# Kernel optimization log

Measured on AMD Instinct MI355X. Metric: run time of the kernel, lower is better.

The kernel has to match this reference:

```python
import jax, jax.numpy as jnp
import numpy as np

H, W = 1024, 2048
PS, ST = 16, 8          # patch_size, stride (init kwargs)
MARGIN = 1e-4           # margin from nerfstudio depth_ranking_loss
NH = (H - PS) // ST + 1  # 127
NW = (W - PS) // ST + 1  # 255
P = NH * NW             # 32385 patches
N = PS * PS             # 256 pixels per patch


def setup_inputs() -> dict:
    key = jax.random.key(0)
    k1, k2, k3, k4 = jax.random.split(key, 4)
    pred = jax.random.normal(k1, (1, 1, H, W), dtype=jnp.float32)
    target = jax.random.normal(k2, (1, 1, H, W), dtype=jnp.float32)
    mask = jax.random.bernoulli(k3, 0.5, (1, 1, H, W))
    # per-patch randomness standing in for torch.randperm: argsort of this
    # noise restricted to valid pixels is a uniform random permutation of
    # the masked (valid) pixel list.
    perm_noise = jax.random.uniform(k4, (P, N), dtype=jnp.float32)
    return {"pred": pred, "target": target, "mask": mask, "perm_noise": perm_noise}


def _extract_patches(x):
    # x: [H, W] -> [P, N] overlapping PSxPS patches with stride ST (scan order)
    i0 = jnp.arange(0, H - PS + 1, ST)           # [NH]
    j0 = jnp.arange(0, W - PS + 1, ST)           # [NW]
    ii = i0[:, None] + jnp.arange(PS)[None, :]   # [NH, PS]
    jj = j0[:, None] + jnp.arange(PS)[None, :]   # [NW, PS]
    g = x[ii[:, None, :, None], jj[None, :, None, :]]  # [NH, NW, PS, PS]
    return g.reshape(P, N)


def reference(pred, target, mask, perm_noise):
    pp = _extract_patches(pred[0, 0])            # [P, N]
    tp = _extract_patches(target[0, 0])          # [P, N]
    mp = _extract_patches(mask[0, 0])            # [P, N] bool

    # rank of each valid pixel in scan order (torch: pred_patch[mask] ordering)
    rank = jnp.cumsum(mp.astype(jnp.int32), axis=1) - 1        # [P, N]
    # random permutation of valid pixels: valid pixels sorted by noise come first
    noise = jnp.where(mp, perm_noise, jnp.inf)
    order = jnp.argsort(noise, axis=1)                          # [P, N]
    # valid pixel with scan-rank r pairs with order[r] (a random valid pixel)
    partner = jnp.take_along_axis(order, jnp.clip(rank, 0, N - 1), axis=1)

    dt = tp - jnp.take_along_axis(tp, partner, axis=1)
    dp = pp - jnp.take_along_axis(pp, partner, axis=1) + MARGIN

    # depth_ranking_loss: penalize pairs whose signs disagree, loss = mean |dp|
    sel = mp & (jnp.sign(dt) != jnp.sign(dp))
    cnt = jnp.sum(sel, axis=1).astype(pp.dtype)                 # [P]
    patch_loss = jnp.sum(jnp.where(sel, jnp.abs(dp), 0.0), axis=1) / cnt

    has_valid = jnp.any(mp, axis=1)                             # skip empty-mask patches
    n_used = jnp.sum(has_valid).astype(pp.dtype)
    return jnp.sum(jnp.where(has_valid, patch_loss, 0.0)) / n_used
```

## Files before the change

### kernel.cpp

```cpp
#include <hip/hip_runtime.h>
#include <cstdint>

#define H 1024
#define W 2048
#define PS 16
#define ST 8
#define NHH ((H - PS) / ST + 1)
#define NWW ((W - PS) / ST + 1)
#define NPATCH (NHH * NWW)
#define NN 256
#define MARGIN 1e-4f
#define RED_BLOCKS 128
#define WPB 4

#define WS_LOSS_OFF   0
#define WS_VALID_OFF  131072
#define WS_ACC_OFF    262144

__global__ void detect_init_kernel(const unsigned int* __restrict__ mw,
                                   unsigned int* __restrict__ wsacc) {
    if (threadIdx.x < 4) wsacc[threadIdx.x] = 0u;
    __syncthreads();
    unsigned int w = mw[threadIdx.x];
    if (w > 1u) atomicOr((int*)(wsacc + 3), 1);
}

__device__ __forceinline__ int resolve_rank(const unsigned* __restrict__ slot,
                                            const unsigned* __restrict__ baseA,
                                            const unsigned* __restrict__ endA,
                                            unsigned key) {
    const unsigned hi = key >> 23;
    const unsigned b  = baseA[hi];
    const unsigned e  = endA[hi];
    int rk = (int)b;
    for (unsigned j = b; j < e; ++j) rk += (int)(slot[j] < key);
    return rk;
}

__global__ __launch_bounds__(256) void patch_loss_kernel(
    const float* __restrict__ pred, const float* __restrict__ target,
    const void* __restrict__ mask, const float* __restrict__ noise,
    const int* __restrict__ byteflag,
    float* __restrict__ out_loss, float* __restrict__ out_valid)
{
    __shared__ float sP[WPB][NN];
    __shared__ float sT[WPB][NN];
    __shared__ unsigned sHist[WPB][NN];
    __shared__ unsigned sBase[WPB][NN];
    __shared__ unsigned sSlot[WPB][NN];
    __shared__ unsigned short sOrder[WPB][NN];

    const int tid  = threadIdx.x;
    const int lane = tid & 63;
    const int wid  = tid >> 6;
    const int p = blockIdx.x * WPB + wid;
    if (p >= NPATCH) return;

    const int ih = p / NWW;
    const int iw = p - ih * NWW;
    const int e0  = lane << 2;
    const int row = e0 >> 4;
    const int col = e0 & 15;
    const int pix = (ih * ST + row) * W + iw * ST + col;

    const float4 pv = *(const float4*)(pred + pix);
    const float4 tv = *(const float4*)(target + pix);
    const float4 nz = *(const float4*)(noise + p * NN + e0);

    int m0, m1, m2, m3;
    if (*byteflag) {
        const unsigned mw_ = *(const unsigned*)((const unsigned char*)mask + pix);
        m0 = (mw_ & 0x000000FFu) != 0; m1 = (mw_ & 0x0000FF00u) != 0;
        m2 = (mw_ & 0x00FF0000u) != 0; m3 = (mw_ & 0xFF000000u) != 0;
    } else {
        const int4 mv = *(const int4*)((const int*)mask + pix);
        m0 = mv.x != 0; m1 = mv.y != 0; m2 = mv.z != 0; m3 = mv.w != 0;
    }
    const int localcnt = m0 + m1 + m2 + m3;

    int incl = localcnt;
#pragma unroll
    for (int d = 1; d < 64; d <<= 1) {
        const int t = __shfl_up(incl, d);
        if (lane >= d) incl += t;
    }
    const int cnt = __shfl(incl, 63);
    const int r0 = incl - localcnt;
    const int r1 = r0 + m0;
    const int r2 = r1 + m1;
    const int r3 = r2 + m2;

    *(float4*)&sP[wid][e0] = pv;
    *(float4*)&sT[wid][e0] = tv;

    const unsigned k0 = ((__float_as_uint(nz.x + 1.0f) - 0x3F800000u) << 8) | (unsigned)(e0 + 0);
    const unsigned k1 = ((__float_as_uint(nz.y + 1.0f) - 0x3F800000u) << 8) | (unsigned)(e0 + 1);
    const unsigned k2 = ((__float_as_uint(nz.z + 1.0f) - 0x3F800000u) << 8) | (unsigned)(e0 + 2);
    const unsigned k3 = ((__float_as_uint(nz.w + 1.0f) - 0x3F800000u) << 8) | (unsigned)(e0 + 3);

    *(uint4*)&sHist[wid][e0] = make_uint4(0u, 0u, 0u, 0u);
    __builtin_amdgcn_wave_barrier();
    if (m0) atomicAdd(&sHist[wid][k0 >> 23], 1u);
    if (m1) atomicAdd(&sHist[wid][k1 >> 23], 1u);
    if (m2) atomicAdd(&sHist[wid][k2 >> 23], 1u);
    if (m3) atomicAdd(&sHist[wid][k3 >> 23], 1u);
    __builtin_amdgcn_wave_barrier();

    const uint4 hq = *(uint4*)&sHist[wid][e0];
    const unsigned lsum = hq.x + hq.y + hq.z + hq.w;
    int hincl = (int)lsum;
#pragma unroll
    for (int d = 1; d < 64; d <<= 1) {
        const int t = __shfl_up(hincl, d);
        if (lane >= d) hincl += t;
    }
    const unsigned b0 = (unsigned)hincl - lsum;
    const unsigned b1 = b0 + hq.x;
    const unsigned b2 = b1 + hq.y;
    const unsigned b3 = b2 + hq.z;
    const uint4 bq = make_uint4(b0, b1, b2, b3);
    *(uint4*)&sHist[wid][e0] = bq;
    *(uint4*)&sBase[wid][e0] = bq;
    __builtin_amdgcn_wave_barrier();

    if (m0) { const unsigned s = atomicAdd(&sHist[wid][k0 >> 23], 1u); sSlot[wid][s] = k0; }
    if (m1) { const unsigned s = atomicAdd(&sHist[wid][k1 >> 23], 1u); sSlot[wid][s] = k1; }
    if (m2) { const unsigned s = atomicAdd(&sHist[wid][k2 >> 23], 1u); sSlot[wid][s] = k2; }
    if (m3) { const unsigned s = atomicAdd(&sHist[wid][k3 >> 23], 1u); sSlot[wid][s] = k3; }
    __builtin_amdgcn_wave_barrier();

    if (m0) sOrder[wid][resolve_rank(sSlot[wid], sBase[wid], sHist[wid], k0)] = (unsigned short)(k0 & 0xFFu);
    if (m1) sOrder[wid][resolve_rank(sSlot[wid], sBase[wid], sHist[wid], k1)] = (unsigned short)(k1 & 0xFFu);
    if (m2) sOrder[wid][resolve_rank(sSlot[wid], sBase[wid], sHist[wid], k2)] = (unsigned short)(k2 & 0xFFu);
    if (m3) sOrder[wid][resolve_rank(sSlot[wid], sBase[wid], sHist[wid], k3)] = (unsigned short)(k3 & 0xFFu);
    __builtin_amdgcn_wave_barrier();

    float la = 0.0f;
    int   lc = 0;
    if (m0) {
        const int pa = sOrder[wid][r0];
        const float dt = tv.x - sT[wid][pa];
        const float dp = pv.x - sP[wid][pa] + MARGIN;
        if (((dt > 0.0f) - (dt < 0.0f)) != ((dp > 0.0f) - (dp < 0.0f))) { la += fabsf(dp); ++lc; }
    }
    if (m1) {
        const int pa = sOrder[wid][r1];
        const float dt = tv.y - sT[wid][pa];
        const float dp = pv.y - sP[wid][pa] + MARGIN;
        if (((dt > 0.0f) - (dt < 0.0f)) != ((dp > 0.0f) - (dp < 0.0f))) { la += fabsf(dp); ++lc; }
    }
    if (m2) {
        const int pa = sOrder[wid][r2];
        const float dt = tv.z - sT[wid][pa];
        const float dp = pv.z - sP[wid][pa] + MARGIN;
        if (((dt > 0.0f) - (dt < 0.0f)) != ((dp > 0.0f) - (dp < 0.0f))) { la += fabsf(dp); ++lc; }
    }
    if (m3) {
        const int pa = sOrder[wid][r3];
        const float dt = tv.w - sT[wid][pa];
        const float dp = pv.w - sP[wid][pa] + MARGIN;
        if (((dt > 0.0f) - (dt < 0.0f)) != ((dp > 0.0f) - (dp < 0.0f))) { la += fabsf(dp); ++lc; }
    }

    float lcf = (float)lc;
#pragma unroll
    for (int off = 32; off > 0; off >>= 1) {
        la  += __shfl_down(la, off);
        lcf += __shfl_down(lcf, off);
    }
    if (lane == 0) {
        float pl = 0.0f, hv = 0.0f;
        if (cnt > 0) { pl = la / lcf; hv = 1.0f; }
        out_loss[p]  = pl;
        out_valid[p] = hv;
    }
}

__global__ __launch_bounds__(256) void reduce_finalize_kernel(
    const float* __restrict__ loss, const float* __restrict__ valid,
    float* __restrict__ acc, unsigned int* __restrict__ ticket,
    float* __restrict__ out)
{
    __shared__ float sa[4], sb[4];
    float a = 0.0f, b = 0.0f;
    for (int i = blockIdx.x * blockDim.x + threadIdx.x; i < NPATCH;
         i += gridDim.x * blockDim.x) {
        a += loss[i];
        b += valid[i];
    }
    for (int off = 32; off > 0; off >>= 1) {
        a += __shfl_down(a, off);
        b += __shfl_down(b, off);
    }
    const int lane = threadIdx.x & 63, wid = threadIdx.x >> 6;
    if (lane == 0) { sa[wid] = a; sb[wid] = b; }
    __syncthreads();
    if (threadIdx.x == 0) {
        atomicAdd(&acc[0], sa[0] + sa[1] + sa[2] + sa[3]);
        atomicAdd(&acc[1], sb[0] + sb[1] + sb[2] + sb[3]);
        __threadfence();
        const unsigned int old = atomicAdd(ticket, 1u);
        if (old == (unsigned int)(gridDim.x - 1)) {
            const float s = atomicAdd(&acc[0], 0.0f);
            const float c = atomicAdd(&acc[1], 0.0f);
            out[0] = s / c;
        }
    }
}

extern "C" void kernel_launch(void* const* d_in, const int* in_sizes, int n_in,
                              void* d_out, int out_size, void* d_ws, size_t ws_size,
                              hipStream_t stream) {
    const float* pred   = (const float*)d_in[0];
    const float* target = (const float*)d_in[1];
    const void*  mask   = d_in[2];
    const float* noise  = (const float*)d_in[3];

    char* ws = (char*)d_ws;
    float*        ws_loss  = (float*)(ws + WS_LOSS_OFF);
    float*        ws_valid = (float*)(ws + WS_VALID_OFF);
    float*        acc      = (float*)(ws + WS_ACC_OFF);
    unsigned int* ticket   = (unsigned int*)(ws + WS_ACC_OFF + 8);
    int*          flag     = (int*)(ws + WS_ACC_OFF + 12);

    const int nblocks = (NPATCH + WPB - 1) / WPB;
    detect_init_kernel<<<1, 1024, 0, stream>>>((const unsigned int*)mask,
                                               (unsigned int*)acc);
    patch_loss_kernel<<<nblocks, 256, 0, stream>>>(pred, target, mask, noise,
                                                   flag, ws_loss, ws_valid);
    reduce_finalize_kernel<<<RED_BLOCKS, 256, 0, stream>>>(ws_loss, ws_valid,
                                                           acc, ticket,
                                                           (float*)d_out);
}
```

Baseline: 118.6 us.

## Fuse per-patch reduction via slotted atomics and pack histogram base/end in shared

```diff
diff --git a/kernel.cpp b/kernel.cpp
--- a/kernel.cpp
+++ b/kernel.cpp
@@ -10,28 +10,28 @@
 #define NPATCH (NHH * NWW)
 #define NN 256
 #define MARGIN 1e-4f
-#define RED_BLOCKS 128
 #define WPB 4
-
-#define WS_LOSS_OFF   0
-#define WS_VALID_OFF  131072
-#define WS_ACC_OFF    262144
+#define NSLOT 128
+#define SLOT_STRIDE 8
+
+#define WS_VALID_F 1024
+#define WS_FLAG_F  2048
 
 __global__ void detect_init_kernel(const unsigned int* __restrict__ mw,
-                                   unsigned int* __restrict__ wsacc) {
-    if (threadIdx.x < 4) wsacc[threadIdx.x] = 0u;
+                                   float* __restrict__ wsf) {
+    ((float2*)wsf)[threadIdx.x] = make_float2(0.0f, 0.0f);
+    if (threadIdx.x == 0) ((int*)wsf)[WS_FLAG_F] = 0;
     __syncthreads();
-    unsigned int w = mw[threadIdx.x];
-    if (w > 1u) atomicOr((int*)(wsacc + 3), 1);
+    const unsigned int w = mw[threadIdx.x];
+    if (w > 1u) atomicOr((int*)wsf + WS_FLAG_F, 1);
 }
 
 __device__ __forceinline__ int resolve_rank(const unsigned* __restrict__ slot,
-                                            const unsigned* __restrict__ baseA,
-                                            const unsigned* __restrict__ endA,
+                                            const unsigned* __restrict__ histp,
                                             unsigned key) {
-    const unsigned hi = key >> 23;
-    const unsigned b  = baseA[hi];
-    const unsigned e  = endA[hi];
+    const unsigned w = histp[key >> 23];
+    const unsigned b = w >> 16;
+    const unsigned e = w & 0xFFFFu;
     int rk = (int)b;
     for (unsigned j = b; j < e; ++j) rk += (int)(slot[j] < key);
     return rk;
@@ -41,12 +41,11 @@
     const float* __restrict__ pred, const float* __restrict__ target,
     const void* __restrict__ mask, const float* __restrict__ noise,
     const int* __restrict__ byteflag,
-    float* __restrict__ out_loss, float* __restrict__ out_valid)
+    float* __restrict__ lossAcc, float* __restrict__ validAcc)
 {
     __shared__ float sP[WPB][NN];
     __shared__ float sT[WPB][NN];
     __shared__ unsigned sHist[WPB][NN];
-    __shared__ unsigned sBase[WPB][NN];
     __shared__ unsigned sSlot[WPB][NN];
     __shared__ unsigned short sOrder[WPB][NN];
 
@@ -118,21 +117,20 @@
     const unsigned b1 = b0 + hq.x;
     const unsigned b2 = b1 + hq.y;
     const unsigned b3 = b2 + hq.z;
-    const uint4 bq = make_uint4(b0, b1, b2, b3);
-    *(uint4*)&sHist[wid][e0] = bq;
-    *(uint4*)&sBase[wid][e0] = bq;
-    __builtin_amdgcn_wave_barrier();
-
-    if (m0) { const unsigned s = atomicAdd(&sHist[wid][k0 >> 23], 1u); sSlot[wid][s] = k0; }
-    if (m1) { const unsigned s = atomicAdd(&sHist[wid][k1 >> 23], 1u); sSlot[wid][s] = k1; }
-    if (m2) { const unsigned s = atomicAdd(&sHist[wid][k2 >> 23], 1u); sSlot[wid][s] = k2; }
-    if (m3) { const unsigned s = atomicAdd(&sHist[wid][k3 >> 23], 1u); sSlot[wid][s] = k3; }
-    __builtin_amdgcn_wave_barrier();
-
-    if (m0) sOrder[wid][resolve_rank(sSlot[wid], sBase[wid], sHist[wid], k0)] = (unsigned short)(k0 & 0xFFu);
-    if (m1) sOrder[wid][resolve_rank(sSlot[wid], sBase[wid], sHist[wid], k1)] = (unsigned short)(k1 & 0xFFu);
-    if (m2) sOrder[wid][resolve_rank(sSlot[wid], sBase[wid], sHist[wid], k2)] = (unsigned short)(k2 & 0xFFu);
-    if (m3) sOrder[wid][resolve_rank(sSlot[wid], sBase[wid], sHist[wid], k3)] = (unsigned short)(k3 & 0xFFu);
+    *(uint4*)&sHist[wid][e0] = make_uint4((b0 << 16) | b0, (b1 << 16) | b1,
+                                          (b2 << 16) | b2, (b3 << 16) | b3);
+    __builtin_amdgcn_wave_barrier();
+
+    if (m0) { const unsigned s = atomicAdd(&sHist[wid][k0 >> 23], 1u) & 0xFFFFu; sSlot[wid][s] = k0; }
+    if (m1) { const unsigned s = atomicAdd(&sHist[wid][k1 >> 23], 1u) & 0xFFFFu; sSlot[wid][s] = k1; }
+    if (m2) { const unsigned s = atomicAdd(&sHist[wid][k2 >> 23], 1u) & 0xFFFFu; sSlot[wid][s] = k2; }
+    if (m3) { const unsigned s = atomicAdd(&sHist[wid][k3 >> 23], 1u) & 0xFFFFu; sSlot[wid][s] = k3; }
+    __builtin_amdgcn_wave_barrier();
+
+    if (m0) sOrder[wid][resolve_rank(sSlot[wid], sHist[wid], k0)] = (unsigned short)(k0 & 0xFFu);
+    if (m1) sOrder[wid][resolve_rank(sSlot[wid], sHist[wid], k1)] = (unsigned short)(k1 & 0xFFu);
+    if (m2) sOrder[wid][resolve_rank(sSlot[wid], sHist[wid], k2)] = (unsigned short)(k2 & 0xFFu);
+    if (m3) sOrder[wid][resolve_rank(sSlot[wid], sHist[wid], k3)] = (unsigned short)(k3 & 0xFFu);
     __builtin_amdgcn_wave_barrier();
 
     float la = 0.0f;
@@ -168,44 +166,25 @@
         la  += __shfl_down(la, off);
         lcf += __shfl_down(lcf, off);
     }
-    if (lane == 0) {
-        float pl = 0.0f, hv = 0.0f;
-        if (cnt > 0) { pl = la / lcf; hv = 1.0f; }
-        out_loss[p]  = pl;
-        out_valid[p] = hv;
-    }
-}
-
-__global__ __launch_bounds__(256) void reduce_finalize_kernel(
-    const float* __restrict__ loss, const float* __restrict__ valid,
-    float* __restrict__ acc, unsigned int* __restrict__ ticket,
-    float* __restrict__ out)
-{
-    __shared__ float sa[4], sb[4];
-    float a = 0.0f, b = 0.0f;
-    for (int i = blockIdx.x * blockDim.x + threadIdx.x; i < NPATCH;
-         i += gridDim.x * blockDim.x) {
-        a += loss[i];
-        b += valid[i];
-    }
+    if (lane == 0 && cnt > 0) {
+        const int slot = (p & (NSLOT - 1)) * SLOT_STRIDE;
+        atomicAdd(&lossAcc[slot],  la / lcf);
+        atomicAdd(&validAcc[slot], 1.0f);
+    }
+}
+
+__global__ void finalize_kernel(const float* __restrict__ wsf,
+                                float* __restrict__ out) {
+    const int lane = threadIdx.x;
+    float a = wsf[lane * SLOT_STRIDE] + wsf[(lane + 64) * SLOT_STRIDE];
+    float b = wsf[WS_VALID_F + lane * SLOT_STRIDE]
+            + wsf[WS_VALID_F + (lane + 64) * SLOT_STRIDE];
+#pragma unroll
     for (int off = 32; off > 0; off >>= 1) {
         a += __shfl_down(a, off);
         b += __shfl_down(b, off);
     }
-    const int lane = threadIdx.x & 63, wid = threadIdx.x >> 6;
-    if (lane == 0) { sa[wid] = a; sb[wid] = b; }
-    __syncthreads();
-    if (threadIdx.x == 0) {
-        atomicAdd(&acc[0], sa[0] + sa[1] + sa[2] + sa[3]);
-        atomicAdd(&acc[1], sb[0] + sb[1] + sb[2] + sb[3]);
-        __threadfence();
-        const unsigned int old = atomicAdd(ticket, 1u);
-        if (old == (unsigned int)(gridDim.x - 1)) {
-            const float s = atomicAdd(&acc[0], 0.0f);
-            const float c = atomicAdd(&acc[1], 0.0f);
-            out[0] = s / c;
-        }
-    }
+    if (lane == 0) out[0] = a / b;
 }
 
 extern "C" void kernel_launch(void* const* d_in, const int* in_sizes, int n_in,
@@ -216,19 +195,14 @@
     const void*  mask   = d_in[2];
     const float* noise  = (const float*)d_in[3];
 
-    char* ws = (char*)d_ws;
-    float*        ws_loss  = (float*)(ws + WS_LOSS_OFF);
-    float*        ws_valid = (float*)(ws + WS_VALID_OFF);
-    float*        acc      = (float*)(ws + WS_ACC_OFF);
-    unsigned int* ticket   = (unsigned int*)(ws + WS_ACC_OFF + 8);
-    int*          flag     = (int*)(ws + WS_ACC_OFF + 12);
+    float* wsf      = (float*)d_ws;
+    float* lossAcc  = wsf;
+    float* validAcc = wsf + WS_VALID_F;
+    int*   flag     = (int*)wsf + WS_FLAG_F;
 
     const int nblocks = (NPATCH + WPB - 1) / WPB;
-    detect_init_kernel<<<1, 1024, 0, stream>>>((const unsigned int*)mask,
-                                               (unsigned int*)acc);
+    detect_init_kernel<<<1, 1024, 0, stream>>>((const unsigned int*)mask, wsf);
     patch_loss_kernel<<<nblocks, 256, 0, stream>>>(pred, target, mask, noise,
-                                                   flag, ws_loss, ws_valid);
-    reduce_finalize_kernel<<<RED_BLOCKS, 256, 0, stream>>>(ws_loss, ws_valid,
-                                                           acc, ticket,
-                                                           (float*)d_out);
-}
+                                                   flag, lossAcc, validAcc);
+    finalize_kernel<<<1, 64, 0, stream>>>(wsf, (float*)d_out);
+}
```

Measured after the change: 111.7 us. -5.8%, faster.
